# Performance work log

Hardware: AMD Instinct MI355X
Metric: run time of the kernel (lower is better)

## Reference

```python
import jax, jax.numpy as jnp
import numpy as np

TEMP = 0.07
IGNORE = 255
NUM_CLS = 150   # ADE Challenge classes
VOCAB = 512     # size of the dense idx_star -> cls_idx LUT
B, D, H, W = 4, 512, 256, 256


def setup_inputs() -> dict:
    key = jax.random.key(0)
    k1, k2, k3 = jax.random.split(key, 3)
    pred_embs = jax.random.normal(k1, (B, D, H, W), dtype=jnp.float32)
    # class text embeddings, L2-normalized per class (as in load_ade_challenge_info)
    cls = jax.random.normal(k2, (NUM_CLS, D), dtype=jnp.float32)
    cls_embs = cls / jnp.linalg.norm(cls, axis=1, keepdims=True)
    # idx_star semantic label map, shape (B, 1, H, W)
    idx_star_map = jax.random.randint(k3, (B, 1, H, W), 0, VOCAB, dtype=jnp.int32)
    # dense LUT replacing the python dict idx_star2cls_idx:
    # first NUM_CLS idx_star values map to class indices, the rest are ignored (255)
    ar = jnp.arange(VOCAB, dtype=jnp.int32)
    lut = jnp.where(ar < NUM_CLS, ar, IGNORE).astype(jnp.int32)
    return {"pred_embs": pred_embs, "cls_embs": cls_embs,
            "idx_star_map": idx_star_map, "lut": lut}


def reference(pred_embs, cls_embs, idx_star_map, lut):
    # --- label remap: single gather replaces the per-unique-value mask loop ---
    labels = lut[idx_star_map[:, 0]]                       # (B, H, W) int32
    # --- 1x1 conv == per-pixel dot product with class embeddings ---
    sim = jnp.einsum('bdhw,kd->bkhw', pred_embs, cls_embs) / TEMP  # (B, K, H, W)
    # --- cross-entropy with ignore_index=255 (mean over valid pixels) ---
    logp = jax.nn.log_softmax(sim, axis=1)                 # (B, K, H, W)
    valid = labels != IGNORE
    safe = jnp.where(valid, labels, 0)
    nll = -jnp.take_along_axis(logp, safe[:, None], axis=1)[:, 0]  # (B, H, W)
    n_valid = jnp.sum(valid).astype(nll.dtype)
    return jnp.sum(jnp.where(valid, nll, 0.0)) / n_valid
```

## Files before the change

### kernel.cpp

```cpp
#include <hip/hip_runtime.h>
#include <hip/hip_bf16.h>


#define NUM_CLS 150
#define NT_TILES 10
#define D_DIM   512
#define HW_DIM  65536
#define IGNORE_L 255

typedef __attribute__((ext_vector_type(8))) short bf16x8;
typedef __attribute__((ext_vector_type(4))) float f32x4;
typedef __attribute__((ext_vector_type(4))) unsigned int u32x4;

#define GLOAD16(gsrc, ldst) \
    __builtin_amdgcn_global_load_lds((const __attribute__((address_space(1))) void*)(gsrc), \
                                     (__attribute__((address_space(3))) void*)(ldst), 16, 0, 0)

static __device__ __forceinline__ short f2bf(float f) {
    __hip_bfloat16 h = __float2bfloat16(f);
    return __builtin_bit_cast(short, h);
}

__global__ void rsl_pack_cls(const float* __restrict__ cls,
                             unsigned short* __restrict__ packed,
                             double* __restrict__ ws_sum,
                             unsigned long long* __restrict__ ws_cnt)
{
    int t = blockIdx.x * 256 + threadIdx.x;
    if (t == 0) { ws_sum[0] = 0.0; ws_cnt[0] = 0ull; }
    if (t >= 16 * NT_TILES * 64) return;
    int s  = t / (NT_TILES * 64);
    int r  = t - s * (NT_TILES * 64);
    int nt = r >> 6;
    int l  = r & 63;
    int c  = nt * 16 + (l & 15);
    int k  = s * 32 + (l >> 4) * 8;
    unsigned short v[8];
#pragma unroll
    for (int j = 0; j < 8; ++j)
        v[j] = (c < NUM_CLS) ? (unsigned short)f2bf(cls[c * D_DIM + k + j]) : (unsigned short)0;
    u32x4 w;
#pragma unroll
    for (int q = 0; q < 4; ++q)
        w[q] = (unsigned int)v[2 * q] | ((unsigned int)v[2 * q + 1] << 16);
    *(u32x4*)(packed + (size_t)(s * NT_TILES + nt) * 512 + (size_t)l * 8) = w;
}

__global__ __launch_bounds__(256, 2)
void rsl_mfma(const float* __restrict__ pred,
              const unsigned short* __restrict__ packed,
              const int*   __restrict__ idx,
              const int*   __restrict__ lut,
              double* __restrict__ ws_sum,
              unsigned long long* __restrict__ ws_cnt)
{
    __shared__ float          sP[2][32][128];
    __shared__ unsigned short sC[2][NT_TILES][512];

    const int lane = threadIdx.x & 63;
    const int wid  = threadIdx.x >> 6;
    const int row  = lane & 15;
    const int g    = lane >> 4;

    const int pixbase = blockIdx.x * 128;
    const int b  = pixbase >> 16;
    const int p0 = pixbase & 0xFFFF;
    const float* pstage = pred + (size_t)b * D_DIM * HW_DIM
                        + (size_t)(lane >> 5) * HW_DIM + (p0 + (lane & 31) * 4);

    f32x4 acc[2][NT_TILES] = {};

    {
#pragma unroll
        for (int tt = 0; tt < 4; ++tt) {
            const int t = wid * 4 + tt;
            GLOAD16(pstage + (size_t)(2 * t) * HW_DIM, &sP[0][2 * t][0]);
        }
        for (int nt = wid; nt < NT_TILES; nt += 4)
            GLOAD16(packed + (size_t)nt * 512 + (size_t)lane * 8, &sC[0][nt][0]);
    }
    __syncthreads();

    for (int s = 0; s < 16; ++s) {
        const int cur = s & 1;
        if (s < 15) {
            const float* srcb = pstage + (size_t)((s + 1) * 32) * HW_DIM;
#pragma unroll
            for (int tt = 0; tt < 4; ++tt) {
                const int t = wid * 4 + tt;
                GLOAD16(srcb + (size_t)(2 * t) * HW_DIM, &sP[cur ^ 1][2 * t][0]);
            }
            const unsigned short* csrc = packed + (size_t)((s + 1) * NT_TILES) * 512 + (size_t)lane * 8;
            for (int nt = wid; nt < NT_TILES; nt += 4)
                GLOAD16(csrc + (size_t)nt * 512, &sC[cur ^ 1][nt][0]);
        }

        bf16x8 pf[2];
#pragma unroll
        for (int mt = 0; mt < 2; ++mt)
#pragma unroll
            for (int j = 0; j < 8; ++j)
                pf[mt][j] = f2bf(sP[cur][g * 8 + j][wid * 32 + mt * 16 + row]);

#pragma unroll
        for (int nt = 0; nt < NT_TILES; ++nt) {
            bf16x8 cf = *(const bf16x8*)&sC[cur][nt][lane * 8];
#pragma unroll
            for (int mt = 0; mt < 2; ++mt)
                acc[mt][nt] = __builtin_amdgcn_mfma_f32_16x16x32_bf16(pf[mt], cf, acc[mt][nt], 0, 0, 0);
        }
        __syncthreads();
    }

    const float invT = 1.0f / 0.07f;
    float local_sum = 0.f;
    int   local_cnt = 0;
#pragma unroll
    for (int mt = 0; mt < 2; ++mt) {
#pragma unroll
        for (int j = 0; j < 4; ++j) {
            const int pixg = pixbase + wid * 32 + mt * 16 + g * 4 + j;
            const int lab  = lut[idx[pixg]];
            const bool valid = (lab != IGNORE_L);

            float m = -1e30f;
#pragma unroll
            for (int nt = 0; nt < NT_TILES; ++nt) {
                int c = nt * 16 + row;
                float v = (c < NUM_CLS) ? acc[mt][nt][j] : -1e30f;
                m = fmaxf(m, v);
            }
#pragma unroll
            for (int o = 8; o >= 1; o >>= 1) m = fmaxf(m, __shfl_xor(m, o));

            float ssum = 0.f, slab = 0.f;
#pragma unroll
            for (int nt = 0; nt < NT_TILES; ++nt) {
                int c = nt * 16 + row;
                if (c < NUM_CLS) {
                    float v = acc[mt][nt][j];
                    ssum += __expf((v - m) * invT);
                    slab += (c == lab) ? v : 0.f;
                }
            }
#pragma unroll
            for (int o = 8; o >= 1; o >>= 1) {
                ssum += __shfl_xor(ssum, o);
                slab += __shfl_xor(slab, o);
            }
            if (row == 0 && valid) {
                local_sum += (m - slab) * invT + __logf(ssum);
                local_cnt += 1;
            }
        }
    }

#pragma unroll
    for (int o = 32; o >= 1; o >>= 1) {
        local_sum += __shfl_down(local_sum, o);
        local_cnt += __shfl_down(local_cnt, o);
    }
    __shared__ float sv[4];
    __shared__ int   sc[4];
    if (lane == 0) { sv[wid] = local_sum; sc[wid] = local_cnt; }
    __syncthreads();
    if (threadIdx.x == 0) {
        float tv = sv[0] + sv[1] + sv[2] + sv[3];
        int   tc = sc[0] + sc[1] + sc[2] + sc[3];
        atomicAdd(ws_sum, (double)tv);
        atomicAdd(ws_cnt, (unsigned long long)tc);
    }
}

__global__ void rsl_final(const double* __restrict__ ws_sum,
                          const unsigned long long* __restrict__ ws_cnt,
                          float* __restrict__ out)
{
    if (threadIdx.x == 0) {
        double c = (double)ws_cnt[0];
        out[0] = (float)(ws_sum[0] / (c > 0.0 ? c : 1.0));
    }
}

extern "C" void kernel_launch(void* const* d_in, const int* in_sizes, int n_in,
                              void* d_out, int out_size, void* d_ws, size_t ws_size,
                              hipStream_t stream)
{
    const float* pred = (const float*)d_in[0];
    const float* cls  = (const float*)d_in[1];
    const int*   idx  = (const int*)d_in[2];
    const int*   lut  = (const int*)d_in[3];
    float* out = (float*)d_out;

    double* wsd = (double*)d_ws;
    unsigned long long* wsc = (unsigned long long*)((char*)d_ws + 8);
    unsigned short* packed = (unsigned short*)((char*)d_ws + 1024);

    rsl_pack_cls<<<40, 256, 0, stream>>>(cls, packed, wsd, wsc);

    const int total = 4 * HW_DIM;
    rsl_mfma<<<total / 128, 256, 0, stream>>>(pred, packed, idx, lut, wsd, wsc);
    rsl_final<<<1, 64, 0, stream>>>(wsd, wsc, out);
}
```

Baseline: 131.6 us.

## Switch class GEMM to 32x32x16 MFMA tiles and raise occupancy target

Replaces the 16x16x32 bf16 MFMA tiling (two pixel tiles by ten class tiles) with 32x32x16 MFMA over five 32-wide class tiles. The packed class-embedding layout and the softmax epilogue indexing change to match the new lane-to-row/column mapping. This reduces MFMA instruction count and per-wave class-fragment LDS reads. It also raises the launch_bounds occupancy hint from 2 to 3 blocks per CU, which may force register spilling given the 80-float accumulator.

```diff
diff --git a/kernel.cpp b/kernel.cpp
--- a/kernel.cpp
+++ b/kernel.cpp
@@ -3,14 +3,14 @@
 
 
 #define NUM_CLS 150
-#define NT_TILES 10
+#define NT_TILES 5
 #define D_DIM   512
 #define HW_DIM  65536
 #define IGNORE_L 255
 
-typedef __attribute__((ext_vector_type(8))) short bf16x8;
-typedef __attribute__((ext_vector_type(4))) float f32x4;
-typedef __attribute__((ext_vector_type(4))) unsigned int u32x4;
+typedef __attribute__((ext_vector_type(8)))  short bf16x8;
+typedef __attribute__((ext_vector_type(16))) float f32x16;
+typedef __attribute__((ext_vector_type(4)))  unsigned int u32x4;
 
 #define GLOAD16(gsrc, ldst) \
     __builtin_amdgcn_global_load_lds((const __attribute__((address_space(1))) void*)(gsrc), \
@@ -28,13 +28,13 @@
 {
     int t = blockIdx.x * 256 + threadIdx.x;
     if (t == 0) { ws_sum[0] = 0.0; ws_cnt[0] = 0ull; }
-    if (t >= 16 * NT_TILES * 64) return;
-    int s  = t / (NT_TILES * 64);
-    int r  = t - s * (NT_TILES * 64);
+    if (t >= 32 * NT_TILES * 64) return;
+    int s2 = t / (NT_TILES * 64);
+    int r  = t - s2 * (NT_TILES * 64);
     int nt = r >> 6;
     int l  = r & 63;
-    int c  = nt * 16 + (l & 15);
-    int k  = s * 32 + (l >> 4) * 8;
+    int c  = nt * 32 + (l & 31);
+    int k  = s2 * 16 + (l >> 5) * 8;
     unsigned short v[8];
 #pragma unroll
     for (int j = 0; j < 8; ++j)
@@ -43,10 +43,10 @@
 #pragma unroll
     for (int q = 0; q < 4; ++q)
         w[q] = (unsigned int)v[2 * q] | ((unsigned int)v[2 * q + 1] << 16);
-    *(u32x4*)(packed + (size_t)(s * NT_TILES + nt) * 512 + (size_t)l * 8) = w;
+    *(u32x4*)(packed + (size_t)(s2 * NT_TILES + nt) * 512 + (size_t)l * 8) = w;
 }
 
-__global__ __launch_bounds__(256, 2)
+__global__ __launch_bounds__(256, 3)
 void rsl_mfma(const float* __restrict__ pred,
               const unsigned short* __restrict__ packed,
               const int*   __restrict__ idx,
@@ -55,12 +55,12 @@
               unsigned long long* __restrict__ ws_cnt)
 {
     __shared__ float          sP[2][32][128];
-    __shared__ unsigned short sC[2][NT_TILES][512];
+    __shared__ unsigned short sC[2][10][512];
 
     const int lane = threadIdx.x & 63;
     const int wid  = threadIdx.x >> 6;
-    const int row  = lane & 15;
-    const int g    = lane >> 4;
+    const int col  = lane & 31;
+    const int hi   = lane >> 5;
 
     const int pixbase = blockIdx.x * 128;
     const int b  = pixbase >> 16;
@@ -68,17 +68,15 @@
     const float* pstage = pred + (size_t)b * D_DIM * HW_DIM
                         + (size_t)(lane >> 5) * HW_DIM + (p0 + (lane & 31) * 4);
 
-    f32x4 acc[2][NT_TILES] = {};
+    f32x16 acc[NT_TILES] = {};
 
-    {
 #pragma unroll
-        for (int tt = 0; tt < 4; ++tt) {
-            const int t = wid * 4 + tt;
-            GLOAD16(pstage + (size_t)(2 * t) * HW_DIM, &sP[0][2 * t][0]);
-        }
-        for (int nt = wid; nt < NT_TILES; nt += 4)
-            GLOAD16(packed + (size_t)nt * 512 + (size_t)lane * 8, &sC[0][nt][0]);
+    for (int tt = 0; tt < 4; ++tt) {
+        const int t = wid * 4 + tt;
+        GLOAD16(pstage + (size_t)(2 * t) * HW_DIM, &sP[0][2 * t][0]);
     }
+    for (int i = wid; i < 10; i += 4)
+        GLOAD16(packed + (size_t)i * 512 + (size_t)lane * 8, &sC[0][i][0]);
     __syncthreads();
 
     for (int s = 0; s < 16; ++s) {
@@ -90,24 +88,22 @@
                 const int t = wid * 4 + tt;
                 GLOAD16(srcb + (size_t)(2 * t) * HW_DIM, &sP[cur ^ 1][2 * t][0]);
             }
-            const unsigned short* csrc = packed + (size_t)((s + 1) * NT_TILES) * 512 + (size_t)lane * 8;
-            for (int nt = wid; nt < NT_TILES; nt += 4)
-                GLOAD16(csrc + (size_t)nt * 512, &sC[cur ^ 1][nt][0]);
+            const unsigned short* csrc = packed + (size_t)((s + 1) * 10) * 512 + (size_t)lane * 8;
+            for (int i = wid; i < 10; i += 4)
+                GLOAD16(csrc + (size_t)i * 512, &sC[cur ^ 1][i][0]);
         }
 
-        bf16x8 pf[2];
 #pragma unroll
-        for (int mt = 0; mt < 2; ++mt)
+        for (int ks = 0; ks < 2; ++ks) {
+            bf16x8 pf;
 #pragma unroll
             for (int j = 0; j < 8; ++j)
-                pf[mt][j] = f2bf(sP[cur][g * 8 + j][wid * 32 + mt * 16 + row]);
-
+                pf[j] = f2bf(sP[cur][ks * 16 + hi * 8 + j][wid * 32 + col]);
 #pragma unroll
-        for (int nt = 0; nt < NT_TILES; ++nt) {
-            bf16x8 cf = *(const bf16x8*)&sC[cur][nt][lane * 8];
-#pragma unroll
-            for (int mt = 0; mt < 2; ++mt)
-                acc[mt][nt] = __builtin_amdgcn_mfma_f32_16x16x32_bf16(pf[mt], cf, acc[mt][nt], 0, 0, 0);
+            for (int nt = 0; nt < NT_TILES; ++nt) {
+                bf16x8 cf = *(const bf16x8*)&sC[cur][ks * NT_TILES + nt][lane * 8];
+                acc[nt] = __builtin_amdgcn_mfma_f32_32x32x16_bf16(pf, cf, acc[nt], 0, 0, 0);
+            }
         }
         __syncthreads();
     }
@@ -116,42 +112,40 @@
     float local_sum = 0.f;
     int   local_cnt = 0;
 #pragma unroll
-    for (int mt = 0; mt < 2; ++mt) {
+    for (int r = 0; r < 16; ++r) {
+        const int prow = (r & 3) + 8 * (r >> 2) + 4 * hi;
+        const int pixg = pixbase + wid * 32 + prow;
+        const int lab  = lut[idx[pixg]];
+        const bool valid = (lab != IGNORE_L);
+
+        float m = -1e30f;
 #pragma unroll
-        for (int j = 0; j < 4; ++j) {
-            const int pixg = pixbase + wid * 32 + mt * 16 + g * 4 + j;
-            const int lab  = lut[idx[pixg]];
-            const bool valid = (lab != IGNORE_L);
+        for (int nt = 0; nt < NT_TILES; ++nt) {
+            int c = nt * 32 + col;
+            float v = (c < NUM_CLS) ? acc[nt][r] : -1e30f;
+            m = fmaxf(m, v);
+        }
+#pragma unroll
+        for (int o = 16; o >= 1; o >>= 1) m = fmaxf(m, __shfl_xor(m, o));
 
-            float m = -1e30f;
+        float ssum = 0.f, slab = 0.f;
 #pragma unroll
-            for (int nt = 0; nt < NT_TILES; ++nt) {
-                int c = nt * 16 + row;
-                float v = (c < NUM_CLS) ? acc[mt][nt][j] : -1e30f;
-                m = fmaxf(m, v);
+        for (int nt = 0; nt < NT_TILES; ++nt) {
+            int c = nt * 32 + col;
+            if (c < NUM_CLS) {
+                float v = acc[nt][r];
+                ssum += __expf((v - m) * invT);
+                slab += (c == lab) ? v : 0.f;
             }
+        }
 #pragma unroll
-            for (int o = 8; o >= 1; o >>= 1) m = fmaxf(m, __shfl_xor(m, o));
-
-            float ssum = 0.f, slab = 0.f;
-#pragma unroll
-            for (int nt = 0; nt < NT_TILES; ++nt) {
-                int c = nt * 16 + row;
-                if (c < NUM_CLS) {
-                    float v = acc[mt][nt][j];
-                    ssum += __expf((v - m) * invT);
-                    slab += (c == lab) ? v : 0.f;
-                }
-            }
-#pragma unroll
-            for (int o = 8; o >= 1; o >>= 1) {
-                ssum += __shfl_xor(ssum, o);
-                slab += __shfl_xor(slab, o);
-            }
-            if (row == 0 && valid) {
-                local_sum += (m - slab) * invT + __logf(ssum);
-                local_cnt += 1;
-            }
+        for (int o = 16; o >= 1; o >>= 1) {
+            ssum += __shfl_xor(ssum, o);
+            slab += __shfl_xor(slab, o);
+        }
+        if (col == 0 && valid) {
+            local_sum += (m - slab) * invT + __logf(ssum);
+            local_cnt += 1;
         }
     }
 
```

New measurement: 139.5 us. +6.0%, slower.
